# Optimization experiments

Measured on AMD Instinct MI355X. Metric: run time of the kernel, lower is better.

Reference implementation:

```python
import jax, jax.numpy as jnp
import numpy as np

NUM_VARS = 64
LAG = 16
H1 = 64
H2 = 1024
NUM_OUT = 1
BATCH = 16384


def setup_inputs() -> dict:
    key = jax.random.key(0)
    ks = jax.random.split(key, 8)

    def xavier(k, shape, fan_in, fan_out):
        std = float(np.sqrt(2.0 / (fan_in + fan_out)))
        return jax.random.normal(k, shape, dtype=jnp.float32) * std

    inputs = jax.random.normal(ks[0], (BATCH, NUM_VARS * LAG), dtype=jnp.float32)
    # Per-variable sub-network weights, batched over the variable axis.
    W1 = xavier(ks[1], (NUM_VARS, LAG, H1), LAG, H1)
    b1 = jnp.full((NUM_VARS, H1), 0.1, dtype=jnp.float32)
    W2 = xavier(ks[2], (NUM_VARS, H1, H1), H1, H1)
    b2 = jnp.full((NUM_VARS, H1), 0.1, dtype=jnp.float32)
    imp = (jnp.ones((NUM_VARS,), dtype=jnp.float32) / NUM_VARS
           + 1e-5 * jax.random.normal(ks[3], (NUM_VARS,), dtype=jnp.float32))
    W3 = xavier(ks[4], (NUM_VARS * H1, H2), NUM_VARS * H1, H2)
    b3 = jnp.full((H2,), 0.1, dtype=jnp.float32)
    W4 = xavier(ks[5], (H2, NUM_OUT), H2, NUM_OUT)
    b4 = jnp.full((NUM_OUT,), 0.1, dtype=jnp.float32)
    return {"inputs": inputs, "W1": W1, "b1": b1, "W2": W2, "b2": b2,
            "imp": imp, "W3": W3, "b3": b3, "W4": W4, "b4": b4}


def reference(inputs, W1, b1, W2, b2, imp, W3, b3, W4, b4):
    B = inputs.shape[0]
    # [B, V*lag] -> [B, V, lag]; slicing inputs[:, lag*i:lag*(i+1)] == x[:, i, :]
    x = inputs.reshape(B, NUM_VARS, LAG)
    # dp = 0.0 -> dropout is identity
    h = jax.nn.relu(jnp.einsum('bvl,vlh->bvh', x, W1) + b1[None])      # [B, V, H1]
    h = jax.nn.relu(jnp.einsum('bvh,vhk->bvk', h, W2) + b2[None])      # [B, V, H1]
    agg = (h * imp[None, :, None]).reshape(B, NUM_VARS * H1)            # weighted concat
    pred = jax.nn.relu(agg @ W3 + b3) @ W4 + b4                        # [B, NUM_OUT]
    return pred
```

## Files before the change

kernel.cpp:

```cpp
#include <hip/hip_runtime.h>
#include <hip/hip_bf16.h>
#include <stdint.h>

#define B_ROWS 16384
#define NVARS 64
#define LAG 16
#define H1 64
#define H2 1024
#define KDIM (NVARS * H1)

typedef __attribute__((ext_vector_type(8))) short short8;
typedef __attribute__((ext_vector_type(4))) short short4v;
typedef __attribute__((ext_vector_type(4))) float f32x4;

typedef __attribute__((address_space(3))) uint8_t lds_u8;
typedef const __attribute__((address_space(1))) uint8_t glob_u8;

__device__ __forceinline__ void gload_lds16(const void* g, void* l) {
    __builtin_amdgcn_global_load_lds((glob_u8*)g, (lds_u8*)l, 16, 0, 0);
}

__device__ __forceinline__ short f2bf_s(float x) {
    __hip_bfloat16 h = __float2bfloat16(x);
    return *(short*)&h;
}
__device__ __forceinline__ float bf_s2f(short s) {
    __hip_bfloat16 h = *(__hip_bfloat16*)&s;
    return __bfloat162float(h);
}

__global__ __launch_bounds__(256) void convert_w3t_kernel(
    const float* __restrict__ w3, __hip_bfloat16* __restrict__ w3t) {
    __shared__ float tile[64][65];
    const int bx = blockIdx.x;
    const int k0 = (bx >> 4) * 64;
    const int n0 = (bx & 15) * 64;
    const int t = threadIdx.x;
    const int c = t & 63, r0 = t >> 6;
#pragma unroll
    for (int i = 0; i < 16; i++) {
        int r = r0 + i * 4;
        tile[r][c] = w3[(size_t)(k0 + r) * H2 + n0 + c];
    }
    __syncthreads();
#pragma unroll
    for (int i = 0; i < 16; i++) {
        int nr = r0 + i * 4;
        w3t[(size_t)(n0 + nr) * KDIM + k0 + c] = __float2bfloat16(tile[c][nr]);
    }
}

__global__ __launch_bounds__(256) void prep_w12_kernel(
    const float* __restrict__ W1, const float* __restrict__ W2,
    short* __restrict__ w1bh, short* __restrict__ w1bl,
    short* __restrict__ w2bh, short* __restrict__ w2bl) {
    const int v = blockIdx.x, t = threadIdx.x;
    for (int idx = t; idx < 64 * 32; idx += 256) {
        int col = idx >> 5, k = idx & 31;
        float wv = W1[((size_t)v * LAG + (k & 15)) * H1 + col];
        short hi = f2bf_s(wv);
        w1bh[((size_t)v * 64 + col) * 40 + k] = hi;
        w1bl[((size_t)v * 64 + col) * 40 + k] = (k < 16) ? f2bf_s(wv - bf_s2f(hi)) : (short)0;
    }
    for (int idx = t; idx < 64 * 64; idx += 256) {
        int col = idx >> 6, k = idx & 63;
        float wv = W2[((size_t)v * H1 + k) * H1 + col];
        short hi = f2bf_s(wv);
        w2bh[((size_t)v * 64 + col) * 72 + k] = hi;
        w2bl[((size_t)v * 64 + col) * 72 + k] = f2bf_s(wv - bf_s2f(hi));
    }
}

__global__ __launch_bounds__(256) void out_init_kernel(
    const float* __restrict__ b4, float* __restrict__ out) {
    out[blockIdx.x * 256 + threadIdx.x] = b4[0];
}

__global__ __launch_bounds__(256) void subnets_mfma_kernel(
    const float* __restrict__ inputs, const float* __restrict__ b1g,
    const float* __restrict__ b2g, const float* __restrict__ impg,
    const short* __restrict__ w1bh_g, const short* __restrict__ w1bl_g,
    const short* __restrict__ w2bh_g, const short* __restrict__ w2bl_g,
    __hip_bfloat16* __restrict__ agg) {
    const int v = blockIdx.x >> 7;
    const int b0 = (blockIdx.x & 127) * 128;
    const int t = threadIdx.x;
    const int lane = t & 63, wv = t >> 6;
    const int l15 = lane & 15, g = lane >> 4;

    __shared__ __align__(16) char smem[53248];
    short* xsS   = (short*)smem;
    short* w1bhS = (short*)(smem + 10240);
    short* w1blS = (short*)(smem + 15360);
    short* Hs    = (short*)smem;
    short* w2bhS = (short*)(smem + 34816);
    short* w2blS = (short*)(smem + 44032);

    for (int c = t; c < 320; c += 256) {
        gload_lds16(w1bh_g + (size_t)v * 2560 + c * 8, (char*)w1bhS + c * 16);
        gload_lds16(w1bl_g + (size_t)v * 2560 + c * 8, (char*)w1blS + c * 16);
    }
    for (int c = t; c < 576; c += 256) {
        gload_lds16(w2bh_g + (size_t)v * 4608 + c * 8, (char*)w2bhS + c * 16);
        gload_lds16(w2bl_g + (size_t)v * 4608 + c * 8, (char*)w2blS + c * 16);
    }
#pragma unroll
    for (int i = 0; i < 2; i++) {
        int idx = t + i * 256;
        int row = idx >> 2, seg = idx & 3;
        float4 x4 = *(const float4*)(inputs + (size_t)(b0 + row) * (NVARS * LAG) + v * LAG + seg * 4);
        const float* xp = (const float*)&x4;
        short4v hv, lv;
#pragma unroll
        for (int j = 0; j < 4; j++) {
            short hi = f2bf_s(xp[j]);
            hv[j] = hi;
            lv[j] = f2bf_s(xp[j] - bf_s2f(hi));
        }
        *(short4v*)&xsS[row * 40 + seg * 4] = hv;
        *(short4v*)&xsS[row * 40 + 16 + seg * 4] = lv;
    }
    __syncthreads();

    short8 a1[2], b1hF[4], b1lF[4];
#pragma unroll
    for (int mt = 0; mt < 2; mt++)
        a1[mt] = *(const short8*)&xsS[(wv * 32 + mt * 16 + l15) * 40 + g * 8];
#pragma unroll
    for (int nt = 0; nt < 4; nt++) {
        b1hF[nt] = *(const short8*)&w1bhS[(nt * 16 + l15) * 40 + g * 8];
        b1lF[nt] = *(const short8*)&w1blS[(nt * 16 + l15) * 40 + g * 8];
    }
    f32x4 acc1[2][4];
#pragma unroll
    for (int mt = 0; mt < 2; mt++)
#pragma unroll
        for (int nt = 0; nt < 4; nt++) {
            acc1[mt][nt] = (f32x4){0.f, 0.f, 0.f, 0.f};
            acc1[mt][nt] = __builtin_amdgcn_mfma_f32_16x16x32_bf16(a1[mt], b1hF[nt], acc1[mt][nt], 0, 0, 0);
            acc1[mt][nt] = __builtin_amdgcn_mfma_f32_16x16x32_bf16(a1[mt], b1lF[nt], acc1[mt][nt], 0, 0, 0);
        }
    __syncthreads();

#pragma unroll
    for (int mt = 0; mt < 2; mt++)
#pragma unroll
        for (int nt = 0; nt < 4; nt++) {
            int col = nt * 16 + l15;
            float bias = b1g[v * H1 + col];
#pragma unroll
            for (int r = 0; r < 4; r++) {
                float h = fmaxf(acc1[mt][nt][r] + bias, 0.f);
                short hi = f2bf_s(h);
                short lo = f2bf_s(h - bf_s2f(hi));
                int row = wv * 32 + mt * 16 + g * 4 + r;
                Hs[row * 136 + col] = hi;
                Hs[row * 136 + 64 + col] = lo;
            }
        }
    __syncthreads();

    short8 a2[2][4], b2hF[4][2], b2lF[4][2];
#pragma unroll
    for (int mt = 0; mt < 2; mt++)
#pragma unroll
        for (int c = 0; c < 4; c++)
            a2[mt][c] = *(const short8*)&Hs[(wv * 32 + mt * 16 + l15) * 136 + c * 32 + g * 8];
#pragma unroll
    for (int nt = 0; nt < 4; nt++)
#pragma unroll
        for (int kc = 0; kc < 2; kc++) {
            b2hF[nt][kc] = *(const short8*)&w2bhS[(nt * 16 + l15) * 72 + kc * 32 + g * 8];
            b2lF[nt][kc] = *(const short8*)&w2blS[(nt * 16 + l15) * 72 + kc * 32 + g * 8];
        }
    f32x4 acc2[2][4];
#pragma unroll
    for (int mt = 0; mt < 2; mt++)
#pragma unroll
        for (int nt = 0; nt < 4; nt++) {
            f32x4 a = (f32x4){0.f, 0.f, 0.f, 0.f};
            a = __builtin_amdgcn_mfma_f32_16x16x32_bf16(a2[mt][0], b2hF[nt][0], a, 0, 0, 0);
            a = __builtin_amdgcn_mfma_f32_16x16x32_bf16(a2[mt][1], b2hF[nt][1], a, 0, 0, 0);
            a = __builtin_amdgcn_mfma_f32_16x16x32_bf16(a2[mt][2], b2hF[nt][0], a, 0, 0, 0);
            a = __builtin_amdgcn_mfma_f32_16x16x32_bf16(a2[mt][3], b2hF[nt][1], a, 0, 0, 0);
            a = __builtin_amdgcn_mfma_f32_16x16x32_bf16(a2[mt][0], b2lF[nt][0], a, 0, 0, 0);
            a = __builtin_amdgcn_mfma_f32_16x16x32_bf16(a2[mt][1], b2lF[nt][1], a, 0, 0, 0);
            acc2[mt][nt] = a;
        }

    const float impv = impg[v];
#pragma unroll
    for (int mt = 0; mt < 2; mt++)
#pragma unroll
        for (int nt = 0; nt < 4; nt++) {
            int col = nt * 16 + l15;
            float bias = b2g[v * H1 + col];
#pragma unroll
            for (int r = 0; r < 4; r++) {
                float o = fmaxf(acc2[mt][nt][r] + bias, 0.f) * impv;
                int row = b0 + wv * 32 + mt * 16 + g * 4 + r;
                agg[(size_t)row * KDIM + v * H1 + col] = __float2bfloat16(o);
            }
        }
}

#define NT 128

__global__ __launch_bounds__(512, 2) void gemm3_kernel(
    const __hip_bfloat16* __restrict__ agg,
    const __hip_bfloat16* __restrict__ w3t,
    const float* __restrict__ b3, const float* __restrict__ W4,
    float* __restrict__ out) {
    const int bid = ((blockIdx.x & 7) << 5) + (blockIdx.x >> 3);
    const int brow = (bid >> 2) * 256;
    const int bcol = (bid & 3) * 256;
    const int t = threadIdx.x;
    const int lane = t & 63;
    const int wid = t >> 6;
    const int wm = wid >> 2, wn = wid & 3;
    const int l15 = lane & 15, g = lane >> 4;

    __shared__ __align__(16) char smem[65536];

    const int c0 = t, c1 = t + 512;
    const int r0 = c0 >> 2, r1 = c1 >> 2;
    const int col0 = ((c0 & 3) * 8) ^ ((r0 & 8) ? 16 : 0);
    const int col1 = ((c1 & 3) * 8) ^ ((r1 & 8) ? 16 : 0);
    const __hip_bfloat16* aS0 = agg + (size_t)(brow + r0) * KDIM + col0;
    const __hip_bfloat16* aS1 = agg + (size_t)(brow + r1) * KDIM + col1;
    const __hip_bfloat16* bS0 = w3t + (size_t)(bcol + r0) * KDIM + col0;
    const __hip_bfloat16* bS1 = w3t + (size_t)(bcol + r1) * KDIM + col1;

#define STAGE_A(p, kt) do { \
        gload_lds16(aS0 + (kt) * 32, smem + (p) * 16384 + c0 * 16); \
        gload_lds16(aS1 + (kt) * 32, smem + (p) * 16384 + c1 * 16); } while (0)
#define STAGE_B(p, kt) do { \
        gload_lds16(bS0 + (kt) * 32, smem + 32768 + (p) * 16384 + c0 * 16); \
        gload_lds16(bS1 + (kt) * 32, smem + 32768 + (p) * 16384 + c1 * 16); } while (0)

    const int coff = (g * 16) ^ ((l15 & 8) ? 32 : 0);
    const int aBase = (wm * 128 + l15) * 64 + coff;
    const int bBase = 32768 + (wn * 64 + l15) * 64 + coff;

#define LDA(dst, p, m) (dst) = *(const short8*)(smem + (p) * 16384 + aBase + (m) * 1024)
#define LDB(dst, p, n) (dst) = *(const short8*)(smem + (p) * 16384 + bBase + (n) * 1024)

    short8 fa[2][8], fb[2][4];
    f32x4 acc[8][4];
#pragma unroll
    for (int m = 0; m < 8; m++)
#pragma unroll
        for (int n = 0; n < 4; n++) acc[m][n] = (f32x4){0.f, 0.f, 0.f, 0.f};

    STAGE_A(0, 0); STAGE_B(0, 0);
    STAGE_A(1, 1); STAGE_B(1, 1);
    asm volatile("s_waitcnt vmcnt(2)" ::: "memory");
    __builtin_amdgcn_s_barrier();
#pragma unroll
    for (int m = 0; m < 8; m++) LDA(fa[0][m], 0, m);
#pragma unroll
    for (int n = 0; n < 4; n++) LDB(fb[0][n], 0, n);
    asm volatile("s_waitcnt lgkmcnt(0)" ::: "memory");
    __builtin_amdgcn_s_barrier();

#define PHASE(tt, CUR, NXT, MB) \
    { \
        const int tn_ = (tt) + 1; \
        if (tn_ < NT) { \
            const int p_ = tn_ & 1; \
            if ((MB) == 0) { \
                LDA(fa[NXT][0], p_, 0); LDA(fa[NXT][1], p_, 1); \
                LDA(fa[NXT][2], p_, 2); LDA(fa[NXT][3], p_, 3); \
                LDA(fa[NXT][4], p_, 4); LDA(fa[NXT][5], p_, 5); \
            } else { \
                LDA(fa[NXT][6], p_, 6); LDA(fa[NXT][7], p_, 7); \
                LDB(fb[NXT][0], p_, 0); LDB(fb[NXT][1], p_, 1); \
                LDB(fb[NXT][2], p_, 2); LDB(fb[NXT][3], p_, 3); \
            } \
        } \
        if ((tt) + 2 < NT) { \
            if ((MB) == 0) STAGE_A((tt) & 1, (tt) + 2); \
            else           STAGE_B((tt) & 1, (tt) + 2); \
            asm volatile("s_waitcnt vmcnt(2)" ::: "memory"); \
        } else { \
            asm volatile("s_waitcnt vmcnt(0)" ::: "memory"); \
        } \
        __builtin_amdgcn_s_barrier(); \
        asm volatile("s_waitcnt lgkmcnt(0)" ::: "memory"); \
        __builtin_amdgcn_sched_barrier(0); \
        __builtin_amdgcn_s_setprio(1); \
        _Pragma("unroll") \
        for (int mm = 0; mm < 4; mm++) \
            _Pragma("unroll") \
            for (int nn = 0; nn < 4; nn++) \
                acc[(MB) + mm][nn] = __builtin_amdgcn_mfma_f32_16x16x32_bf16( \
                    fa[CUR][(MB) + mm], fb[CUR][nn], acc[(MB) + mm][nn], 0, 0, 0); \
        __builtin_amdgcn_s_setprio(0); \
        __builtin_amdgcn_s_barrier(); \
    }

    for (int t2 = 0; t2 < NT / 2; t2++) {
        const int tt = t2 * 2;
        PHASE(tt,     0, 1, 0)
        PHASE(tt,     0, 1, 4)
        PHASE(tt + 1, 1, 0, 0)
        PHASE(tt + 1, 1, 0, 4)
    }

    float bias[4], w4v[4];
#pragma unroll
    for (int n = 0; n < 4; n++) {
        int col = bcol + wn * 64 + n * 16 + l15;
        bias[n] = b3[col];
        w4v[n] = W4[col];
    }
#pragma unroll
    for (int m = 0; m < 8; m++) {
        float pr0 = 0.f, pr1 = 0.f, pr2 = 0.f, pr3 = 0.f;
#pragma unroll
        for (int n = 0; n < 4; n++) {
            pr0 += fmaxf(acc[m][n][0] + bias[n], 0.f) * w4v[n];
            pr1 += fmaxf(acc[m][n][1] + bias[n], 0.f) * w4v[n];
            pr2 += fmaxf(acc[m][n][2] + bias[n], 0.f) * w4v[n];
            pr3 += fmaxf(acc[m][n][3] + bias[n], 0.f) * w4v[n];
        }
#pragma unroll
        for (int mask = 1; mask < 16; mask <<= 1) {
            pr0 += __shfl_xor(pr0, mask, 64);
            pr1 += __shfl_xor(pr1, mask, 64);
            pr2 += __shfl_xor(pr2, mask, 64);
            pr3 += __shfl_xor(pr3, mask, 64);
        }
        if (l15 == 0) {
            int row = brow + wm * 128 + m * 16 + g * 4;
            atomicAdd(&out[row + 0], pr0);
            atomicAdd(&out[row + 1], pr1);
            atomicAdd(&out[row + 2], pr2);
            atomicAdd(&out[row + 3], pr3);
        }
    }
}

extern "C" void kernel_launch(void* const* d_in, const int* in_sizes, int n_in,
                              void* d_out, int out_size, void* d_ws, size_t ws_size,
                              hipStream_t stream) {
    const float* inputs = (const float*)d_in[0];
    const float* W1 = (const float*)d_in[1];
    const float* b1 = (const float*)d_in[2];
    const float* W2 = (const float*)d_in[3];
    const float* b2 = (const float*)d_in[4];
    const float* imp = (const float*)d_in[5];
    const float* W3 = (const float*)d_in[6];
    const float* b3 = (const float*)d_in[7];
    const float* W4 = (const float*)d_in[8];
    const float* b4 = (const float*)d_in[9];
    float* out = (float*)d_out;

    char* ws = (char*)d_ws;
    const size_t agg_bytes  = (size_t)B_ROWS * KDIM * 2;
    const size_t w3t_bytes  = (size_t)H2 * KDIM * 2;
    const size_t w1b_bytes  = (size_t)NVARS * 64 * 40 * 2;
    const size_t w2b_bytes  = (size_t)NVARS * 64 * 72 * 2;

    __hip_bfloat16* agg = (__hip_bfloat16*)ws;
    __hip_bfloat16* w3t = (__hip_bfloat16*)(ws + agg_bytes);
    short* w1bh = (short*)(ws + agg_bytes + w3t_bytes);
    short* w1bl = (short*)(ws + agg_bytes + w3t_bytes + w1b_bytes);
    short* w2bh = (short*)(ws + agg_bytes + w3t_bytes + 2 * w1b_bytes);
    short* w2bl = (short*)(ws + agg_bytes + w3t_bytes + 2 * w1b_bytes + w2b_bytes);

    hipLaunchKernelGGL(convert_w3t_kernel, dim3(1024), dim3(256), 0, stream, W3, w3t);
    hipLaunchKernelGGL(prep_w12_kernel, dim3(NVARS), dim3(256), 0, stream,
                       W1, W2, w1bh, w1bl, w2bh, w2bl);
    hipLaunchKernelGGL(out_init_kernel, dim3(B_ROWS / 256), dim3(256), 0, stream, b4, out);
    hipLaunchKernelGGL(subnets_mfma_kernel, dim3(NVARS * (B_ROWS / 128)), dim3(256), 0, stream,
                       inputs, b1, b2, imp, w1bh, w1bl, w2bh, w2bl, agg);
    hipLaunchKernelGGL(gemm3_kernel, dim3((B_ROWS / 256) * (H2 / 256)), dim3(512), 0, stream,
                       agg, w3t, b3, W4, out);
}
```

Before: 184.8 us.

## Deepen GEMM3 LDS pipeline to four stages and drop register fragment double-buffering

Grows the shared-memory ring from two to four K-tile stages (128 KB), with global-to-LDS prefetch running three tiles ahead and vmcnt waits adjusted to match. A and B for each stage now share one 32 KB slot. The register-level double-buffering of A/B fragments is removed: each half-phase loads its fragments from LDS and then runs MFMAs on them. The aim is to hide global-load latency better, but the larger LDS footprint likely allows fewer resident blocks per CU, and LDS read latency is no longer overlapped with MFMA work.

```diff
diff --git a/kernel.cpp b/kernel.cpp
--- a/kernel.cpp
+++ b/kernel.cpp
@@ -220,7 +220,7 @@
     const int wm = wid >> 2, wn = wid & 3;
     const int l15 = lane & 15, g = lane >> 4;
 
-    __shared__ __align__(16) char smem[65536];
+    __shared__ __align__(16) char smem[131072];
 
     const int c0 = t, c1 = t + 512;
     const int r0 = c0 >> 2, r1 = c1 >> 2;
@@ -232,20 +232,20 @@
     const __hip_bfloat16* bS1 = w3t + (size_t)(bcol + r1) * KDIM + col1;
 
 #define STAGE_A(p, kt) do { \
-        gload_lds16(aS0 + (kt) * 32, smem + (p) * 16384 + c0 * 16); \
-        gload_lds16(aS1 + (kt) * 32, smem + (p) * 16384 + c1 * 16); } while (0)
+        gload_lds16(aS0 + (kt) * 32, smem + (p) * 32768 + c0 * 16); \
+        gload_lds16(aS1 + (kt) * 32, smem + (p) * 32768 + c1 * 16); } while (0)
 #define STAGE_B(p, kt) do { \
-        gload_lds16(bS0 + (kt) * 32, smem + 32768 + (p) * 16384 + c0 * 16); \
-        gload_lds16(bS1 + (kt) * 32, smem + 32768 + (p) * 16384 + c1 * 16); } while (0)
+        gload_lds16(bS0 + (kt) * 32, smem + (p) * 32768 + 16384 + c0 * 16); \
+        gload_lds16(bS1 + (kt) * 32, smem + (p) * 32768 + 16384 + c1 * 16); } while (0)
 
     const int coff = (g * 16) ^ ((l15 & 8) ? 32 : 0);
     const int aBase = (wm * 128 + l15) * 64 + coff;
-    const int bBase = 32768 + (wn * 64 + l15) * 64 + coff;
-
-#define LDA(dst, p, m) (dst) = *(const short8*)(smem + (p) * 16384 + aBase + (m) * 1024)
-#define LDB(dst, p, n) (dst) = *(const short8*)(smem + (p) * 16384 + bBase + (n) * 1024)
-
-    short8 fa[2][8], fb[2][4];
+    const int bBase = 16384 + (wn * 64 + l15) * 64 + coff;
+
+#define LDA(i, p) fa[i] = *(const short8*)(smem + (p) * 32768 + aBase + (i) * 1024)
+#define LDB(i, p) fb[i] = *(const short8*)(smem + (p) * 32768 + bBase + (i) * 1024)
+
+    short8 fa[8], fb[4];
     f32x4 acc[8][4];
 #pragma unroll
     for (int m = 0; m < 8; m++)
@@ -254,37 +254,14 @@
 
     STAGE_A(0, 0); STAGE_B(0, 0);
     STAGE_A(1, 1); STAGE_B(1, 1);
-    asm volatile("s_waitcnt vmcnt(2)" ::: "memory");
+    STAGE_A(2, 2); STAGE_B(2, 2);
+    asm volatile("s_waitcnt vmcnt(8)" ::: "memory");
     __builtin_amdgcn_s_barrier();
-#pragma unroll
-    for (int m = 0; m < 8; m++) LDA(fa[0][m], 0, m);
-#pragma unroll
-    for (int n = 0; n < 4; n++) LDB(fb[0][n], 0, n);
-    asm volatile("s_waitcnt lgkmcnt(0)" ::: "memory");
-    __builtin_amdgcn_s_barrier();
-
-#define PHASE(tt, CUR, NXT, MB) \
-    { \
-        const int tn_ = (tt) + 1; \
-        if (tn_ < NT) { \
-            const int p_ = tn_ & 1; \
-            if ((MB) == 0) { \
-                LDA(fa[NXT][0], p_, 0); LDA(fa[NXT][1], p_, 1); \
-                LDA(fa[NXT][2], p_, 2); LDA(fa[NXT][3], p_, 3); \
-                LDA(fa[NXT][4], p_, 4); LDA(fa[NXT][5], p_, 5); \
-            } else { \
-                LDA(fa[NXT][6], p_, 6); LDA(fa[NXT][7], p_, 7); \
-                LDB(fb[NXT][0], p_, 0); LDB(fb[NXT][1], p_, 1); \
-                LDB(fb[NXT][2], p_, 2); LDB(fb[NXT][3], p_, 3); \
-            } \
-        } \
-        if ((tt) + 2 < NT) { \
-            if ((MB) == 0) STAGE_A((tt) & 1, (tt) + 2); \
-            else           STAGE_B((tt) & 1, (tt) + 2); \
-            asm volatile("s_waitcnt vmcnt(2)" ::: "memory"); \
-        } else { \
-            asm volatile("s_waitcnt vmcnt(0)" ::: "memory"); \
-        } \
+
+#define PH_A(p, DOSTAGE, kt3) do { \
+        LDA(0, p); LDA(1, p); LDA(2, p); LDA(3, p); \
+        LDB(0, p); LDB(1, p); LDB(2, p); LDB(3, p); \
+        if (DOSTAGE) STAGE_A((kt3) & 3, kt3); \
         __builtin_amdgcn_s_barrier(); \
         asm volatile("s_waitcnt lgkmcnt(0)" ::: "memory"); \
         __builtin_amdgcn_sched_barrier(0); \
@@ -293,19 +270,38 @@
         for (int mm = 0; mm < 4; mm++) \
             _Pragma("unroll") \
             for (int nn = 0; nn < 4; nn++) \
-                acc[(MB) + mm][nn] = __builtin_amdgcn_mfma_f32_16x16x32_bf16( \
-                    fa[CUR][(MB) + mm], fb[CUR][nn], acc[(MB) + mm][nn], 0, 0, 0); \
+                acc[mm][nn] = __builtin_amdgcn_mfma_f32_16x16x32_bf16( \
+                    fa[mm], fb[nn], acc[mm][nn], 0, 0, 0); \
         __builtin_amdgcn_s_setprio(0); \
+        __builtin_amdgcn_s_barrier(); } while (0)
+
+#define PH_B(p, DOSTAGE, kt3, VMSTR) do { \
+        LDA(4, p); LDA(5, p); LDA(6, p); LDA(7, p); \
+        if (DOSTAGE) STAGE_B((kt3) & 3, kt3); \
+        asm volatile(VMSTR ::: "memory"); \
         __builtin_amdgcn_s_barrier(); \
-    }
-
-    for (int t2 = 0; t2 < NT / 2; t2++) {
-        const int tt = t2 * 2;
-        PHASE(tt,     0, 1, 0)
-        PHASE(tt,     0, 1, 4)
-        PHASE(tt + 1, 1, 0, 0)
-        PHASE(tt + 1, 1, 0, 4)
-    }
+        asm volatile("s_waitcnt lgkmcnt(0)" ::: "memory"); \
+        __builtin_amdgcn_sched_barrier(0); \
+        __builtin_amdgcn_s_setprio(1); \
+        _Pragma("unroll") \
+        for (int mm = 0; mm < 4; mm++) \
+            _Pragma("unroll") \
+            for (int nn = 0; nn < 4; nn++) \
+                acc[4 + mm][nn] = __builtin_amdgcn_mfma_f32_16x16x32_bf16( \
+                    fa[4 + mm], fb[nn], acc[4 + mm][nn], 0, 0, 0); \
+        __builtin_amdgcn_s_setprio(0); \
+        __builtin_amdgcn_s_barrier(); } while (0)
+
+#pragma unroll 4
+    for (int tt = 0; tt < NT - 4; ++tt) {
+        const int p = tt & 3;
+        PH_A(p, 1, tt + 3);
+        PH_B(p, 1, tt + 3, "s_waitcnt vmcnt(8)");
+    }
+    PH_A(0, 1, 127); PH_B(0, 1, 127, "s_waitcnt vmcnt(8)");
+    PH_A(1, 0, 0);   PH_B(1, 0, 0, "s_waitcnt vmcnt(4)");
+    PH_A(2, 0, 0);   PH_B(2, 0, 0, "s_waitcnt vmcnt(0)");
+    PH_A(3, 0, 0);   PH_B(3, 0, 0, "s_waitcnt vmcnt(0)");
 
     float bias[4], w4v[4];
 #pragma unroll
```

Result: no change. 181.4 us (-1.9%).
